# Optimization experiments

Measured on AMD Instinct MI355X. Metric: run time of the kernel, lower is better.

The kernel has to match this reference:

```python
import math
import jax, jax.numpy as jnp
import numpy as np

B, N, M, C, H = 64, 64, 64, 512, 8
HD = C // H
FREQ = 256  # frequency_embedding_size
MAX_PERIOD = 10000.0


def setup_inputs() -> dict:
    key = jax.random.key(0)
    ks = jax.random.split(key, 10)
    s = 1.0 / math.sqrt(C)
    sf = 1.0 / math.sqrt(FREQ)
    return {
        "query": jax.random.normal(ks[0], (B, N, C), jnp.float32),
        "query_pos": jax.random.uniform(ks[1], (1, N, M), jnp.float32),
        # projection weights stored as [in, out]
        "Wq": jax.random.normal(ks[2], (C, C), jnp.float32) * s,
        "bq": jnp.zeros((C,), jnp.float32),
        "Wk": jax.random.normal(ks[3], (C, C), jnp.float32) * s,  # no bias
        "Wv": jax.random.normal(ks[4], (C, C), jnp.float32) * s,
        "bv": jnp.zeros((C,), jnp.float32),
        "Wo": jax.random.normal(ks[5], (C, C), jnp.float32) * s,
        "bo": jnp.zeros((C,), jnp.float32),
        # ScalarEmbedder MLP: Linear(FREQ->C), SiLU, Linear(C->C)
        "W1": jax.random.normal(ks[6], (FREQ, C), jnp.float32) * sf,
        "b1": jnp.zeros((C,), jnp.float32),
        "W2": jax.random.normal(ks[7], (C, C), jnp.float32) * s,
        "b2": jnp.zeros((C,), jnp.float32),
    }


def _freqs():
    half = FREQ // 2
    return jnp.exp(-math.log(MAX_PERIOD) * jnp.arange(half, dtype=jnp.float32) / half)


def reference(query, query_pos, Wq, bq, Wk, Wv, bv, Wo, bo, W1, b1, W2, b2):
    Bq, Nq, Cq = query.shape
    Mk = query_pos.shape[-1]
    # --- ScalarEmbedder on flattened pairwise positions: [N*M] -> [N*M, C]
    t = query_pos.reshape(-1)                       # [Bp*N*M], Bp = 1
    tf = t[:, None] * _freqs()[None, :]             # [N*M, FREQ/2]
    emb = jnp.concatenate([jnp.cos(tf), jnp.sin(tf)], axis=-1)  # [N*M, FREQ]
    pe = jax.nn.silu(emb @ W1 + b1) @ W2 + b2        # [N*M, C]
    pe = pe.reshape(Nq, Mk, H, HD).transpose(2, 0, 1, 3)  # [H, N, M, hd] (tiled over B via broadcast)

    q = (query @ Wq + bq).reshape(Bq, Nq, H, HD)     # bnhd
    k = (query @ Wk).reshape(Bq, Mk, H, HD)          # bmhd (key = query)
    v = (query @ Wv + bv).reshape(Bq, Mk, H, HD)

    scale = HD ** -0.5
    # attn[b,h,n,m] = sum_d q[b,n,h,d] * pe[h,n,m,d] * k[b,m,h,d]
    scores = jnp.einsum("bnhd,hnmd,bmhd->bhnm", q, pe, k) * scale
    attn = jax.nn.softmax(scores, axis=-1)
    x = jnp.einsum("bhnm,bmhd->bnhd", attn, v).reshape(Bq, Nq, Cq)
    return x @ Wo + bo + query  # identity = query
```

## Files before the change

### kernel.cpp

```cpp
#include <hip/hip_runtime.h>
#include <hip/hip_bf16.h>
#include <math.h>

typedef short short8 __attribute__((ext_vector_type(8)));
typedef float floatx4 __attribute__((ext_vector_type(4)));

__device__ __forceinline__ ushort f2bf(float f) {
    __hip_bfloat16 h = __float2bfloat16(f);
    return *reinterpret_cast<ushort*>(&h);
}
__device__ __forceinline__ void bf8_to_f32(uint4 u, float* f) {
    f[0] = __uint_as_float(u.x << 16); f[1] = __uint_as_float(u.x & 0xffff0000u);
    f[2] = __uint_as_float(u.y << 16); f[3] = __uint_as_float(u.y & 0xffff0000u);
    f[4] = __uint_as_float(u.z << 16); f[5] = __uint_as_float(u.z & 0xffff0000u);
    f[6] = __uint_as_float(u.w << 16); f[7] = __uint_as_float(u.w & 0xffff0000u);
}

#define GLDS16(g, l) __builtin_amdgcn_global_load_lds( \
    (const __attribute__((address_space(1))) void*)(g), \
    (__attribute__((address_space(3))) void*)(l), 16, 0, 0)

__global__ __launch_bounds__(256) void prep_kernel(
        const float* __restrict__ W1, const float* __restrict__ W2,
        const float* __restrict__ Wq, const float* __restrict__ Wk,
        const float* __restrict__ Wv, const float* __restrict__ Wo,
        const float* __restrict__ bq, const float* __restrict__ bv,
        const float* __restrict__ query, const float* __restrict__ qpos,
        ushort* __restrict__ W1t, ushort* __restrict__ W2t,
        ushort* __restrict__ Wqkvt, ushort* __restrict__ Wot,
        ushort* __restrict__ queryB, ushort* __restrict__ embB,
        float* __restrict__ biasC) {
    const int z = blockIdx.z;
    const int tx = threadIdx.x, ty = threadIdx.y;
    const int tid = ty * 32 + tx;
    if (z < 6) {
        const float* src; ushort* dst; int R;
        switch (z) {
            case 0:  src = W1; dst = W1t;              R = 256; break;
            case 1:  src = W2; dst = W2t;              R = 512; break;
            case 2:  src = Wq; dst = Wqkvt;            R = 512; break;
            case 3:  src = Wk; dst = Wqkvt + 512*512;  R = 512; break;
            case 4:  src = Wv; dst = Wqkvt + 1024*512; R = 512; break;
            default: src = Wo; dst = Wot;              R = 512; break;
        }
        const int r0 = blockIdx.y * 32, c0 = blockIdx.x * 32;
        if (r0 >= R) return;
        __shared__ float t[32][33];
        for (int i = ty; i < 32; i += 8) t[i][tx] = src[(size_t)(r0 + i) * 512 + c0 + tx];
        __syncthreads();
        for (int i = ty; i < 32; i += 8) dst[(size_t)(c0 + i) * R + r0 + tx] = f2bf(t[tx][i]);
    } else if (z == 6) {
        const int bid = blockIdx.y * 16 + blockIdx.x;
#pragma unroll
        for (int i = 0; i < 8; ++i) {
            size_t idx4 = (size_t)bid * 2048 + i * 256 + tid;
            float4 v = *(const float4*)(query + idx4 * 4);
            ushort4 o; o.x = f2bf(v.x); o.y = f2bf(v.y); o.z = f2bf(v.z); o.w = f2bf(v.w);
            *(ushort4*)(queryB + idx4 * 4) = o;
        }
        if (bid == 0) {
            for (int i = tid; i < 1536; i += 256)
                biasC[i] = (i < 512) ? bq[i] : ((i < 1024) ? 0.0f : bv[i - 1024]);
        }
    } else {
        const int bid = blockIdx.y * 16 + blockIdx.x;
        const int gt = bid * 256 + tid;
        const int e0 = gt * 16;
        const int r = e0 >> 8, j0 = e0 & 255;
        const float t = qpos[r];
        ushort o[16];
#pragma unroll
        for (int u = 0; u < 16; ++u) {
            int j = j0 + u, i = j & 127;
            float freq = __expf(-9.210340371976184f * (float)i * (1.0f / 128.0f));
            float a = t * freq;
            o[u] = f2bf((j < 128) ? __cosf(a) : __sinf(a));
        }
        *(uint4*)(embB + e0)     = *(uint4*)&o[0];
        *(uint4*)(embB + e0 + 8) = *(uint4*)&o[8];
    }
}

template<int BM, int BN>
__global__ __launch_bounds__(256) void gemm_bf16(
        const ushort* __restrict__ A, const ushort* __restrict__ Bt,
        const float* __restrict__ bias, const float* __restrict__ resid,
        void* __restrict__ Cout, int M, int N, int K, int act, int out_fp32) {
    constexpr int MR = BM / 32;
    constexpr int NR = BN / 32;
    __shared__ ushort As[BM * 32];
    __shared__ ushort Bs[BN * 32];
    const int tid = threadIdx.x;
    const int l = tid & 63, w = tid >> 6;
    const int wr = w >> 1, wc = w & 1;
    const int row0 = blockIdx.x * BM, col0 = blockIdx.y * BN;
    const int l15 = l & 15, quad = l >> 4;

    const int srow = tid >> 2;
    const int skoff = (tid & 3) * 8;
    const ushort* gA = A  + (size_t)(row0 + srow) * K + skoff;
    const ushort* gB = Bt + (size_t)(col0 + srow) * K + skoff;

    floatx4 acc[MR][NR] = {};

    for (int k0 = 0; k0 < K; k0 += 32) {
        __syncthreads();
#pragma unroll
        for (int i = 0; i < BM / 64; ++i)
            GLDS16(gA + (size_t)(i * 64) * K + k0, &As[(i * 256 + tid) * 8]);
#pragma unroll
        for (int i = 0; i < BN / 64; ++i)
            GLDS16(gB + (size_t)(i * 64) * K + k0, &Bs[(i * 256 + tid) * 8]);
        __syncthreads();
        short8 af[MR], bf[NR];
#pragma unroll
        for (int m = 0; m < MR; ++m)
            af[m] = *(const short8*)&As[(wr * (BM / 2) + m * 16 + l15) * 32 + quad * 8];
#pragma unroll
        for (int n = 0; n < NR; ++n)
            bf[n] = *(const short8*)&Bs[(wc * (BN / 2) + n * 16 + l15) * 32 + quad * 8];
#pragma unroll
        for (int m = 0; m < MR; ++m)
#pragma unroll
            for (int n = 0; n < NR; ++n)
                acc[m][n] = __builtin_amdgcn_mfma_f32_16x16x32_bf16(af[m], bf[n], acc[m][n], 0, 0, 0);
    }

#pragma unroll
    for (int m = 0; m < MR; ++m)
#pragma unroll
        for (int n = 0; n < NR; ++n) {
            int col = col0 + wc * (BN / 2) + n * 16 + l15;
            float bvv = bias ? bias[col] : 0.0f;
#pragma unroll
            for (int r = 0; r < 4; ++r) {
                int row = row0 + wr * (BM / 2) + m * 16 + quad * 4 + r;
                float val = acc[m][n][r] + bvv;
                if (act) val = val / (1.0f + __expf(-val));
                if (out_fp32) {
                    float rv = resid ? resid[(size_t)row * N + col] : 0.0f;
                    ((float*)Cout)[(size_t)row * N + col] = val + rv;
                } else {
                    ((ushort*)Cout)[(size_t)row * N + col] = f2bf(val);
                }
            }
        }
}

__global__ __launch_bounds__(256) void attn_bf16(
        const ushort* __restrict__ qkv, const ushort* __restrict__ peB,
        ushort* __restrict__ xB) {
    const int h = blockIdx.x, b = blockIdx.y, nh = blockIdx.z;
    const int tid = threadIdx.x;
    const int w = tid >> 6, l = tid & 63;
    const int lo = l & 7, hi = l >> 3;

    __shared__ float ks[64 * 64];
    __shared__ float vs[64 * 64];
    __shared__ float qs[32 * 64];

#pragma unroll
    for (int p = 0; p < 2; ++p) {
        int cid = p * 256 + tid;
        int row = cid >> 3, ch = cid & 7;
        const ushort* base = qkv + (size_t)(b * 64 + row) * 1536 + h * 64 + ch * 8;
        uint4 ku = *(const uint4*)(base + 512);
        uint4 vu = *(const uint4*)(base + 1024);
        float kf[8], vf[8];
        bf8_to_f32(ku, kf); bf8_to_f32(vu, vf);
#pragma unroll
        for (int j = 0; j < 8; ++j) {
            ks[row * 64 + ch * 8 + j] = kf[j];
            vs[row * 64 + ch * 8 + j] = vf[j];
        }
    }
    {
        int row = tid >> 3, ch = tid & 7;
        uint4 qu = *(const uint4*)(qkv + (size_t)(b * 64 + nh * 32 + row) * 1536 + h * 64 + ch * 8);
        float qf[8]; bf8_to_f32(qu, qf);
#pragma unroll
        for (int j = 0; j < 8; ++j) qs[row * 64 + ch * 8 + j] = qf[j];
    }
    __syncthreads();

    for (int i = 0; i < 8; ++i) {
        int nl = w + 4 * i;
        int n = nh * 32 + nl;
        float qf[8];
        *(float4*)&qf[0] = *(const float4*)&qs[nl * 64 + lo * 8];
        *(float4*)&qf[4] = *(const float4*)&qs[nl * 64 + lo * 8 + 4];

        float sreg[8];
#pragma unroll
        for (int mg = 0; mg < 8; ++mg) {
            int m = mg * 8 + hi;
            uint4 pu = *(const uint4*)(peB + (size_t)(n * 64 + m) * 512 + h * 64 + lo * 8);
            float pf[8]; bf8_to_f32(pu, pf);
            float kf[8];
            *(float4*)&kf[0] = *(const float4*)&ks[m * 64 + lo * 8];
            *(float4*)&kf[4] = *(const float4*)&ks[m * 64 + lo * 8 + 4];
            float p = 0.0f;
#pragma unroll
            for (int j = 0; j < 8; ++j) p = fmaf(qf[j] * kf[j], pf[j], p);
            p += __shfl_xor(p, 1);
            p += __shfl_xor(p, 2);
            p += __shfl_xor(p, 4);
            sreg[mg] = p * 0.125f;
        }

        float mx = sreg[0];
#pragma unroll
        for (int mg = 1; mg < 8; ++mg) mx = fmaxf(mx, sreg[mg]);
        mx = fmaxf(mx, __shfl_xor(mx, 8));
        mx = fmaxf(mx, __shfl_xor(mx, 16));
        mx = fmaxf(mx, __shfl_xor(mx, 32));
        float sum = 0.0f;
#pragma unroll
        for (int mg = 0; mg < 8; ++mg) { sreg[mg] = __expf(sreg[mg] - mx); sum += sreg[mg]; }
        sum += __shfl_xor(sum, 8);
        sum += __shfl_xor(sum, 16);
        sum += __shfl_xor(sum, 32);
        float rs = 1.0f / sum;

        float acc[8] = {};
#pragma unroll
        for (int mg = 0; mg < 8; ++mg) {
            int m = mg * 8 + hi;
            float at = sreg[mg] * rs;
            float vf[8];
            *(float4*)&vf[0] = *(const float4*)&vs[m * 64 + lo * 8];
            *(float4*)&vf[4] = *(const float4*)&vs[m * 64 + lo * 8 + 4];
#pragma unroll
            for (int j = 0; j < 8; ++j) acc[j] = fmaf(at, vf[j], acc[j]);
        }
#pragma unroll
        for (int j = 0; j < 8; ++j) {
            acc[j] += __shfl_xor(acc[j], 8);
            acc[j] += __shfl_xor(acc[j], 16);
            acc[j] += __shfl_xor(acc[j], 32);
        }
        if (l < 8) {
            uint4 o;
            o.x = f2bf(acc[0]) | ((uint)f2bf(acc[1]) << 16);
            o.y = f2bf(acc[2]) | ((uint)f2bf(acc[3]) << 16);
            o.z = f2bf(acc[4]) | ((uint)f2bf(acc[5]) << 16);
            o.w = f2bf(acc[6]) | ((uint)f2bf(acc[7]) << 16);
            *(uint4*)(xB + (size_t)(b * 64 + n) * 512 + h * 64 + l * 8) = o;
        }
    }
}

extern "C" void kernel_launch(void* const* d_in, const int* in_sizes, int n_in,
                              void* d_out, int out_size, void* d_ws, size_t ws_size,
                              hipStream_t stream) {
    const float* query = (const float*)d_in[0];
    const float* qpos  = (const float*)d_in[1];
    const float* Wq    = (const float*)d_in[2];
    const float* bq    = (const float*)d_in[3];
    const float* Wk    = (const float*)d_in[4];
    const float* Wv    = (const float*)d_in[5];
    const float* bv    = (const float*)d_in[6];
    const float* Wo    = (const float*)d_in[7];
    const float* bo    = (const float*)d_in[8];
    const float* W1    = (const float*)d_in[9];
    const float* b1    = (const float*)d_in[10];
    const float* W2    = (const float*)d_in[11];
    const float* b2    = (const float*)d_in[12];
    float* out = (float*)d_out;
    char* ws = (char*)d_ws;

    ushort* W1t    = (ushort*)(ws + 0);
    ushort* W2t    = (ushort*)(ws + 262144);
    ushort* Wqkvt  = (ushort*)(ws + 786432);
    ushort* Wot    = (ushort*)(ws + 2359296);
    float*  biasC  = (float*) (ws + 2883584);
    ushort* embB   = (ushort*)(ws + 3145728);
    ushort* queryB = (ushort*)(ws + 5242880);
    ushort* hiddenB= (ushort*)(ws + 9437184);
    ushort* peB    = (ushort*)(ws + 13631488);
    ushort* qkvB   = (ushort*)(ws + 17825792);
    ushort* xB     = (ushort*)(ws + 30408704);

    prep_kernel<<<dim3(16, 16, 8), dim3(32, 8), 0, stream>>>(
        W1, W2, Wq, Wk, Wv, Wo, bq, bv, query, qpos,
        W1t, W2t, Wqkvt, Wot, queryB, embB, biasC);

    gemm_bf16<128, 64><<<dim3(32, 8),  256, 0, stream>>>(embB,    W1t,   b1,    nullptr, hiddenB, 4096,  512, 256, 1, 0);
    gemm_bf16<128, 64><<<dim3(32, 8),  256, 0, stream>>>(hiddenB, W2t,   b2,    nullptr, peB,     4096,  512, 512, 0, 0);
    gemm_bf16<128,128><<<dim3(32, 12), 256, 0, stream>>>(queryB,  Wqkvt, biasC, nullptr, qkvB,    4096, 1536, 512, 0, 0);

    attn_bf16<<<dim3(8, 64, 2), 256, 0, stream>>>(qkvB, peB, xB);

    gemm_bf16<128, 64><<<dim3(32, 8),  256, 0, stream>>>(xB, Wot, bo, query, out, 4096, 512, 512, 0, 1);
}
```

Before: 183.7 us.

## Double-buffer GEMM LDS tiles and co-launch W2 and QKV GEMMs in one grid

Replaces the GEMM kernel with a multi-problem variant whose K loop double-buffers the LDS tiles. The next tile's global-to-LDS load is issued before the MFMAs on the current tile, so only one barrier is needed per iteration. The independent W2 (positional MLP) and QKV projection GEMMs are merged into a single 1024-block launch selected by block index, which fills the GPU better and removes one launch. The QKV GEMM now uses 128x64 tiles instead of 128x128, and LDS use doubles for the second buffer.

```diff
diff --git a/kernel.cpp b/kernel.cpp
--- a/kernel.cpp
+++ b/kernel.cpp
@@ -81,49 +81,65 @@
     }
 }
 
+struct GArgs {
+    const ushort* A; const ushort* Bt; const float* bias; const float* resid;
+    void* C; int N, K, act, outf32, ntn;
+};
+
 template<int BM, int BN>
-__global__ __launch_bounds__(256) void gemm_bf16(
-        const ushort* __restrict__ A, const ushort* __restrict__ Bt,
-        const float* __restrict__ bias, const float* __restrict__ resid,
-        void* __restrict__ Cout, int M, int N, int K, int act, int out_fp32) {
+__global__ __launch_bounds__(256) void gemm_multi(GArgs g0, GArgs g1, int split) {
     constexpr int MR = BM / 32;
     constexpr int NR = BN / 32;
-    __shared__ ushort As[BM * 32];
-    __shared__ ushort Bs[BN * 32];
+    __shared__ ushort As[2][BM * 32];
+    __shared__ ushort Bs[2][BN * 32];
+
+    const bool sel = ((int)blockIdx.x >= split);
+    const GArgs g = sel ? g1 : g0;
+    const int bid = sel ? ((int)blockIdx.x - split) : (int)blockIdx.x;
+    const int tm = bid / g.ntn, tn = bid % g.ntn;
+    const int row0 = tm * BM, col0 = tn * BN;
+    const int K = g.K, N = g.N;
+
     const int tid = threadIdx.x;
     const int l = tid & 63, w = tid >> 6;
     const int wr = w >> 1, wc = w & 1;
-    const int row0 = blockIdx.x * BM, col0 = blockIdx.y * BN;
     const int l15 = l & 15, quad = l >> 4;
 
     const int srow = tid >> 2;
     const int skoff = (tid & 3) * 8;
-    const ushort* gA = A  + (size_t)(row0 + srow) * K + skoff;
-    const ushort* gB = Bt + (size_t)(col0 + srow) * K + skoff;
+    const ushort* gA = g.A  + (size_t)(row0 + srow) * K + skoff;
+    const ushort* gB = g.Bt + (size_t)(col0 + srow) * K + skoff;
+
+    auto stage = [&](int s, int k0) {
+#pragma unroll
+        for (int i = 0; i < BM / 64; ++i)
+            GLDS16(gA + (size_t)(i * 64) * K + k0, &As[s][(i * 256 + tid) * 8]);
+#pragma unroll
+        for (int i = 0; i < BN / 64; ++i)
+            GLDS16(gB + (size_t)(i * 64) * K + k0, &Bs[s][(i * 256 + tid) * 8]);
+    };
 
     floatx4 acc[MR][NR] = {};
 
-    for (int k0 = 0; k0 < K; k0 += 32) {
+    const int nk = K >> 5;
+    stage(0, 0);
+    int cur = 0;
+    for (int t = 0; t < nk; ++t) {
         __syncthreads();
-#pragma unroll
-        for (int i = 0; i < BM / 64; ++i)
-            GLDS16(gA + (size_t)(i * 64) * K + k0, &As[(i * 256 + tid) * 8]);
-#pragma unroll
-        for (int i = 0; i < BN / 64; ++i)
-            GLDS16(gB + (size_t)(i * 64) * K + k0, &Bs[(i * 256 + tid) * 8]);
-        __syncthreads();
+        if (t + 1 < nk) stage(cur ^ 1, (t + 1) * 32);
         short8 af[MR], bf[NR];
 #pragma unroll
         for (int m = 0; m < MR; ++m)
-            af[m] = *(const short8*)&As[(wr * (BM / 2) + m * 16 + l15) * 32 + quad * 8];
+            af[m] = *(const short8*)&As[cur][(wr * (BM / 2) + m * 16 + l15) * 32 + quad * 8];
 #pragma unroll
         for (int n = 0; n < NR; ++n)
-            bf[n] = *(const short8*)&Bs[(wc * (BN / 2) + n * 16 + l15) * 32 + quad * 8];
+            bf[n] = *(const short8*)&Bs[cur][(wc * (BN / 2) + n * 16 + l15) * 32 + quad * 8];
 #pragma unroll
         for (int m = 0; m < MR; ++m)
 #pragma unroll
             for (int n = 0; n < NR; ++n)
                 acc[m][n] = __builtin_amdgcn_mfma_f32_16x16x32_bf16(af[m], bf[n], acc[m][n], 0, 0, 0);
+        cur ^= 1;
     }
 
 #pragma unroll
@@ -131,17 +147,17 @@
 #pragma unroll
         for (int n = 0; n < NR; ++n) {
             int col = col0 + wc * (BN / 2) + n * 16 + l15;
-            float bvv = bias ? bias[col] : 0.0f;
+            float bvv = g.bias ? g.bias[col] : 0.0f;
 #pragma unroll
             for (int r = 0; r < 4; ++r) {
                 int row = row0 + wr * (BM / 2) + m * 16 + quad * 4 + r;
                 float val = acc[m][n][r] + bvv;
-                if (act) val = val / (1.0f + __expf(-val));
-                if (out_fp32) {
-                    float rv = resid ? resid[(size_t)row * N + col] : 0.0f;
-                    ((float*)Cout)[(size_t)row * N + col] = val + rv;
+                if (g.act) val = val / (1.0f + __expf(-val));
+                if (g.outf32) {
+                    float rv = g.resid ? g.resid[(size_t)row * N + col] : 0.0f;
+                    ((float*)g.C)[(size_t)row * N + col] = val + rv;
                 } else {
-                    ((ushort*)Cout)[(size_t)row * N + col] = f2bf(val);
+                    ((ushort*)g.C)[(size_t)row * N + col] = f2bf(val);
                 }
             }
         }
@@ -285,11 +301,15 @@
         W1, W2, Wq, Wk, Wv, Wo, bq, bv, query, qpos,
         W1t, W2t, Wqkvt, Wot, queryB, embB, biasC);
 
-    gemm_bf16<128, 64><<<dim3(32, 8),  256, 0, stream>>>(embB,    W1t,   b1,    nullptr, hiddenB, 4096,  512, 256, 1, 0);
-    gemm_bf16<128, 64><<<dim3(32, 8),  256, 0, stream>>>(hiddenB, W2t,   b2,    nullptr, peB,     4096,  512, 512, 0, 0);
-    gemm_bf16<128,128><<<dim3(32, 12), 256, 0, stream>>>(queryB,  Wqkvt, biasC, nullptr, qkvB,    4096, 1536, 512, 0, 0);
+    GArgs a_g1 { embB,    W1t,   b1,    nullptr, hiddenB, 512,  256, 1, 0, 8  };
+    GArgs a_g2 { hiddenB, W2t,   b2,    nullptr, peB,     512,  512, 0, 0, 8  };
+    GArgs a_qkv{ queryB,  Wqkvt, biasC, nullptr, qkvB,    1536, 512, 0, 0, 24 };
+    GArgs a_out{ xB,      Wot,   bo,    query,   out,     512,  512, 0, 1, 8  };
+
+    gemm_multi<128, 64><<<256, 256, 0, stream>>>(a_g1, a_g1, 1 << 30);
+    gemm_multi<128, 64><<<1024, 256, 0, stream>>>(a_g2, a_qkv, 256);
 
     attn_bf16<<<dim3(8, 64, 2), 256, 0, stream>>>(qkvB, peB, xB);
 
-    gemm_bf16<128, 64><<<dim3(32, 8),  256, 0, stream>>>(xB, Wot, bo, query, out, 4096, 512, 512, 0, 1);
-}
+    gemm_multi<128, 64><<<256, 256, 0, stream>>>(a_out, a_out, 1 << 30);
+}
```

New measurement: 171.2 us. 1.07x faster.

## Fuse all stages into one persistent kernel with grid barriers

Applied to the files above, without the earlier changes.

Replaces the six separate launches with a single persistent kernel of 512 blocks that walks through the prep, GEMM, attention and output stages, separated by atomic-counter grid barriers. It also overlaps the W1 GEMM with the QKV GEMM in one phase, double-buffers the GEMM K-loop LDS staging, pads the attention LDS rows and prefetches the pe loads. The aim is to remove launch gaps and idle tails between stages. In exchange, the grid barriers require all 512 blocks to be co-resident, some stages switch to smaller 64x64 tiles, and a memset is added before the launch.

```diff
diff --git a/kernel.cpp b/kernel.cpp
--- a/kernel.cpp
+++ b/kernel.cpp
@@ -4,6 +4,8 @@
 
 typedef short short8 __attribute__((ext_vector_type(8)));
 typedef float floatx4 __attribute__((ext_vector_type(4)));
+
+#define NBLK 512
 
 __device__ __forceinline__ ushort f2bf(float f) {
     __hip_bfloat16 h = __float2bfloat16(f);
@@ -20,80 +22,101 @@
     (const __attribute__((address_space(1))) void*)(g), \
     (__attribute__((address_space(3))) void*)(l), 16, 0, 0)
 
-__global__ __launch_bounds__(256) void prep_kernel(
-        const float* __restrict__ W1, const float* __restrict__ W2,
-        const float* __restrict__ Wq, const float* __restrict__ Wk,
-        const float* __restrict__ Wv, const float* __restrict__ Wo,
-        const float* __restrict__ bq, const float* __restrict__ bv,
-        const float* __restrict__ query, const float* __restrict__ qpos,
-        ushort* __restrict__ W1t, ushort* __restrict__ W2t,
-        ushort* __restrict__ Wqkvt, ushort* __restrict__ Wot,
-        ushort* __restrict__ queryB, ushort* __restrict__ embB,
-        float* __restrict__ biasC) {
-    const int z = blockIdx.z;
-    const int tx = threadIdx.x, ty = threadIdx.y;
-    const int tid = ty * 32 + tx;
-    if (z < 6) {
-        const float* src; ushort* dst; int R;
-        switch (z) {
-            case 0:  src = W1; dst = W1t;              R = 256; break;
-            case 1:  src = W2; dst = W2t;              R = 512; break;
-            case 2:  src = Wq; dst = Wqkvt;            R = 512; break;
-            case 3:  src = Wk; dst = Wqkvt + 512*512;  R = 512; break;
-            case 4:  src = Wv; dst = Wqkvt + 1024*512; R = 512; break;
-            default: src = Wo; dst = Wot;              R = 512; break;
-        }
-        const int r0 = blockIdx.y * 32, c0 = blockIdx.x * 32;
-        if (r0 >= R) return;
-        __shared__ float t[32][33];
-        for (int i = ty; i < 32; i += 8) t[i][tx] = src[(size_t)(r0 + i) * 512 + c0 + tx];
-        __syncthreads();
-        for (int i = ty; i < 32; i += 8) dst[(size_t)(c0 + i) * R + r0 + tx] = f2bf(t[tx][i]);
-    } else if (z == 6) {
-        const int bid = blockIdx.y * 16 + blockIdx.x;
-#pragma unroll
-        for (int i = 0; i < 8; ++i) {
-            size_t idx4 = (size_t)bid * 2048 + i * 256 + tid;
-            float4 v = *(const float4*)(query + idx4 * 4);
-            ushort4 o; o.x = f2bf(v.x); o.y = f2bf(v.y); o.z = f2bf(v.z); o.w = f2bf(v.w);
-            *(ushort4*)(queryB + idx4 * 4) = o;
-        }
-        if (bid == 0) {
-            for (int i = tid; i < 1536; i += 256)
-                biasC[i] = (i < 512) ? bq[i] : ((i < 1024) ? 0.0f : bv[i - 1024]);
-        }
-    } else {
-        const int bid = blockIdx.y * 16 + blockIdx.x;
-        const int gt = bid * 256 + tid;
-        const int e0 = gt * 16;
-        const int r = e0 >> 8, j0 = e0 & 255;
-        const float t = qpos[r];
-        ushort o[16];
-#pragma unroll
-        for (int u = 0; u < 16; ++u) {
-            int j = j0 + u, i = j & 127;
-            float freq = __expf(-9.210340371976184f * (float)i * (1.0f / 128.0f));
-            float a = t * freq;
-            o[u] = f2bf((j < 128) ? __cosf(a) : __sinf(a));
-        }
-        *(uint4*)(embB + e0)     = *(uint4*)&o[0];
-        *(uint4*)(embB + e0 + 8) = *(uint4*)&o[8];
-    }
+__device__ __forceinline__ void gbar(uint* cnt, uint target) {
+    __syncthreads();
+    __threadfence();
+    if (threadIdx.x == 0) {
+        __hip_atomic_fetch_add(cnt, 1u, __ATOMIC_ACQ_REL, __HIP_MEMORY_SCOPE_AGENT);
+        uint v;
+        do {
+            __builtin_amdgcn_s_sleep(1);
+            v = __hip_atomic_load(cnt, __ATOMIC_ACQUIRE, __HIP_MEMORY_SCOPE_AGENT);
+        } while (v < target);
+    }
+    __syncthreads();
+    __threadfence();
+}
+
+struct FusedArgs {
+    const float *W1, *W2, *Wq, *Wk, *Wv, *Wo, *bq, *bv, *bo, *b1, *b2;
+    const float *query, *qpos;
+    ushort *W1t, *W2t, *Wqkvt, *Wot, *queryB, *embB;
+    float *biasC;
+    ushort *hiddenB, *peB, *qkvB, *xB;
+    float *out;
+    uint *bars;
+};
+
+__device__ void transpose_task(int t, const FusedArgs& a, char* smem) {
+    const float* src; ushort* dst; int R, z, by, bx;
+    if (t < 128) { z = 0; by = t >> 4; bx = t & 15; }
+    else { int u = t - 128; z = 1 + (u >> 8); int idx = u & 255; by = idx >> 4; bx = idx & 15; }
+    switch (z) {
+        case 0:  src = a.W1; dst = a.W1t;                R = 256; break;
+        case 1:  src = a.W2; dst = a.W2t;                R = 512; break;
+        case 2:  src = a.Wq; dst = a.Wqkvt;              R = 512; break;
+        case 3:  src = a.Wk; dst = a.Wqkvt + 512 * 512;  R = 512; break;
+        case 4:  src = a.Wv; dst = a.Wqkvt + 1024 * 512; R = 512; break;
+        default: src = a.Wo; dst = a.Wot;                R = 512; break;
+    }
+    const int r0 = by * 32, c0 = bx * 32;
+    const int tid = threadIdx.x;
+    const int tx = tid & 31, ty = tid >> 5;
+    float* tt = (float*)smem;
+    __syncthreads();
+    for (int i = ty; i < 32; i += 8) tt[i * 33 + tx] = src[(size_t)(r0 + i) * 512 + c0 + tx];
+    __syncthreads();
+    for (int i = ty; i < 32; i += 8) dst[(size_t)(c0 + i) * R + r0 + tx] = f2bf(tt[tx * 33 + i]);
+}
+
+__device__ void qcast_task(int bid, const FusedArgs& a) {
+    const int tid = threadIdx.x;
+#pragma unroll
+    for (int i = 0; i < 8; ++i) {
+        size_t idx4 = (size_t)bid * 2048 + i * 256 + tid;
+        float4 v = *(const float4*)(a.query + idx4 * 4);
+        ushort4 o; o.x = f2bf(v.x); o.y = f2bf(v.y); o.z = f2bf(v.z); o.w = f2bf(v.w);
+        *(ushort4*)(a.queryB + idx4 * 4) = o;
+    }
+    if (bid == 0) {
+        for (int i = tid; i < 1536; i += 256)
+            a.biasC[i] = (i < 512) ? a.bq[i] : ((i < 1024) ? 0.0f : a.bv[i - 1024]);
+    }
+}
+
+__device__ void emb_task(int bid, const FusedArgs& a) {
+    const int tid = threadIdx.x;
+    const int gt = bid * 256 + tid;
+    const int e0 = gt * 16;
+    const int r = e0 >> 8, j0 = e0 & 255;
+    const float t = a.qpos[r];
+    ushort o[16];
+#pragma unroll
+    for (int u = 0; u < 16; ++u) {
+        int j = j0 + u, i = j & 127;
+        float freq = __expf(-9.210340371976184f * (float)i * (1.0f / 128.0f));
+        float ang = t * freq;
+        o[u] = f2bf((j < 128) ? __cosf(ang) : __sinf(ang));
+    }
+    *(uint4*)(a.embB + e0)     = *(uint4*)&o[0];
+    *(uint4*)(a.embB + e0 + 8) = *(uint4*)&o[8];
 }
 
 template<int BM, int BN>
-__global__ __launch_bounds__(256) void gemm_bf16(
-        const ushort* __restrict__ A, const ushort* __restrict__ Bt,
-        const float* __restrict__ bias, const float* __restrict__ resid,
-        void* __restrict__ Cout, int M, int N, int K, int act, int out_fp32) {
+__device__ void gemm_tile(const ushort* __restrict__ A, const ushort* __restrict__ Bt,
+                          const float* __restrict__ bias, const float* __restrict__ resid,
+                          void* __restrict__ Cout, int N, int K, int act, int outf32,
+                          int ntn, int bid, char* smem) {
     constexpr int MR = BM / 32;
     constexpr int NR = BN / 32;
-    __shared__ ushort As[BM * 32];
-    __shared__ ushort Bs[BN * 32];
+    ushort* As = (ushort*)smem;
+    ushort* Bs = As + 2 * BM * 32;
+    const int tm = bid / ntn, tn = bid % ntn;
+    const int row0 = tm * BM, col0 = tn * BN;
+
     const int tid = threadIdx.x;
     const int l = tid & 63, w = tid >> 6;
     const int wr = w >> 1, wc = w & 1;
-    const int row0 = blockIdx.x * BM, col0 = blockIdx.y * BN;
     const int l15 = l & 15, quad = l >> 4;
 
     const int srow = tid >> 2;
@@ -101,29 +124,38 @@
     const ushort* gA = A  + (size_t)(row0 + srow) * K + skoff;
     const ushort* gB = Bt + (size_t)(col0 + srow) * K + skoff;
 
+    auto stage = [&](int s, int k0) {
+#pragma unroll
+        for (int i = 0; i < BM / 64; ++i)
+            GLDS16(gA + (size_t)(i * 64) * K + k0, &As[(size_t)s * BM * 32 + (i * 256 + tid) * 8]);
+#pragma unroll
+        for (int i = 0; i < BN / 64; ++i)
+            GLDS16(gB + (size_t)(i * 64) * K + k0, &Bs[(size_t)s * BN * 32 + (i * 256 + tid) * 8]);
+    };
+
     floatx4 acc[MR][NR] = {};
-
-    for (int k0 = 0; k0 < K; k0 += 32) {
+    const int nk = K >> 5;
+    __syncthreads();
+    stage(0, 0);
+    int cur = 0;
+    for (int t = 0; t < nk; ++t) {
         __syncthreads();
-#pragma unroll
-        for (int i = 0; i < BM / 64; ++i)
-            GLDS16(gA + (size_t)(i * 64) * K + k0, &As[(i * 256 + tid) * 8]);
-#pragma unroll
-        for (int i = 0; i < BN / 64; ++i)
-            GLDS16(gB + (size_t)(i * 64) * K + k0, &Bs[(i * 256 + tid) * 8]);
-        __syncthreads();
+        if (t + 1 < nk) stage(cur ^ 1, (t + 1) * 32);
+        const ushort* Ab = As + (size_t)cur * BM * 32;
+        const ushort* Bb = Bs + (size_t)cur * BN * 32;
         short8 af[MR], bf[NR];
 #pragma unroll
         for (int m = 0; m < MR; ++m)
-            af[m] = *(const short8*)&As[(wr * (BM / 2) + m * 16 + l15) * 32 + quad * 8];
+            af[m] = *(const short8*)&Ab[(wr * (BM / 2) + m * 16 + l15) * 32 + quad * 8];
 #pragma unroll
         for (int n = 0; n < NR; ++n)
-            bf[n] = *(const short8*)&Bs[(wc * (BN / 2) + n * 16 + l15) * 32 + quad * 8];
+            bf[n] = *(const short8*)&Bb[(wc * (BN / 2) + n * 16 + l15) * 32 + quad * 8];
 #pragma unroll
         for (int m = 0; m < MR; ++m)
 #pragma unroll
             for (int n = 0; n < NR; ++n)
                 acc[m][n] = __builtin_amdgcn_mfma_f32_16x16x32_bf16(af[m], bf[n], acc[m][n], 0, 0, 0);
+        cur ^= 1;
     }
 
 #pragma unroll
@@ -137,7 +169,7 @@
                 int row = row0 + wr * (BM / 2) + m * 16 + quad * 4 + r;
                 float val = acc[m][n][r] + bvv;
                 if (act) val = val / (1.0f + __expf(-val));
-                if (out_fp32) {
+                if (outf32) {
                     float rv = resid ? resid[(size_t)row * N + col] : 0.0f;
                     ((float*)Cout)[(size_t)row * N + col] = val + rv;
                 } else {
@@ -147,18 +179,17 @@
         }
 }
 
-__global__ __launch_bounds__(256) void attn_bf16(
-        const ushort* __restrict__ qkv, const ushort* __restrict__ peB,
-        ushort* __restrict__ xB) {
-    const int h = blockIdx.x, b = blockIdx.y, nh = blockIdx.z;
+__device__ void attn_unit(const ushort* __restrict__ qkv, const ushort* __restrict__ peB,
+                          ushort* __restrict__ xB, int h, int b, int nh, char* smem) {
+    constexpr int LP = 68;
+    float* ks = (float*)smem;
+    float* vs = ks + 64 * LP;
+    float* qs = vs + 64 * LP;
     const int tid = threadIdx.x;
     const int w = tid >> 6, l = tid & 63;
     const int lo = l & 7, hi = l >> 3;
 
-    __shared__ float ks[64 * 64];
-    __shared__ float vs[64 * 64];
-    __shared__ float qs[32 * 64];
-
+    __syncthreads();
 #pragma unroll
     for (int p = 0; p < 2; ++p) {
         int cid = p * 256 + tid;
@@ -170,8 +201,8 @@
         bf8_to_f32(ku, kf); bf8_to_f32(vu, vf);
 #pragma unroll
         for (int j = 0; j < 8; ++j) {
-            ks[row * 64 + ch * 8 + j] = kf[j];
-            vs[row * 64 + ch * 8 + j] = vf[j];
+            ks[row * LP + ch * 8 + j] = kf[j];
+            vs[row * LP + ch * 8 + j] = vf[j];
         }
     }
     {
@@ -179,7 +210,7 @@
         uint4 qu = *(const uint4*)(qkv + (size_t)(b * 64 + nh * 32 + row) * 1536 + h * 64 + ch * 8);
         float qf[8]; bf8_to_f32(qu, qf);
 #pragma unroll
-        for (int j = 0; j < 8; ++j) qs[row * 64 + ch * 8 + j] = qf[j];
+        for (int j = 0; j < 8; ++j) qs[row * LP + ch * 8 + j] = qf[j];
     }
     __syncthreads();
 
@@ -187,18 +218,22 @@
         int nl = w + 4 * i;
         int n = nh * 32 + nl;
         float qf[8];
-        *(float4*)&qf[0] = *(const float4*)&qs[nl * 64 + lo * 8];
-        *(float4*)&qf[4] = *(const float4*)&qs[nl * 64 + lo * 8 + 4];
+        *(float4*)&qf[0] = *(const float4*)&qs[nl * LP + lo * 8];
+        *(float4*)&qf[4] = *(const float4*)&qs[nl * LP + lo * 8 + 4];
+
+        uint4 pu[8];
+#pragma unroll
+        for (int mg = 0; mg < 8; ++mg)
+            pu[mg] = *(const uint4*)(peB + (size_t)(n * 64 + mg * 8 + hi) * 512 + h * 64 + lo * 8);
 
         float sreg[8];
 #pragma unroll
         for (int mg = 0; mg < 8; ++mg) {
             int m = mg * 8 + hi;
-            uint4 pu = *(const uint4*)(peB + (size_t)(n * 64 + m) * 512 + h * 64 + lo * 8);
-            float pf[8]; bf8_to_f32(pu, pf);
+            float pf[8]; bf8_to_f32(pu[mg], pf);
             float kf[8];
-            *(float4*)&kf[0] = *(const float4*)&ks[m * 64 + lo * 8];
-            *(float4*)&kf[4] = *(const float4*)&ks[m * 64 + lo * 8 + 4];
+            *(float4*)&kf[0] = *(const float4*)&ks[m * LP + lo * 8];
+            *(float4*)&kf[4] = *(const float4*)&ks[m * LP + lo * 8 + 4];
             float p = 0.0f;
 #pragma unroll
             for (int j = 0; j < 8; ++j) p = fmaf(qf[j] * kf[j], pf[j], p);
@@ -228,8 +263,8 @@
             int m = mg * 8 + hi;
             float at = sreg[mg] * rs;
             float vf[8];
-            *(float4*)&vf[0] = *(const float4*)&vs[m * 64 + lo * 8];
-            *(float4*)&vf[4] = *(const float4*)&vs[m * 64 + lo * 8 + 4];
+            *(float4*)&vf[0] = *(const float4*)&vs[m * LP + lo * 8];
+            *(float4*)&vf[4] = *(const float4*)&vs[m * LP + lo * 8 + 4];
 #pragma unroll
             for (int j = 0; j < 8; ++j) acc[j] = fmaf(at, vf[j], acc[j]);
         }
@@ -250,46 +285,76 @@
     }
 }
 
+__global__ __launch_bounds__(256, 2) void fused_all(FusedArgs a) {
+    __shared__ __align__(16) char smem[43520];
+    const int blk = blockIdx.x;
+
+    for (int task = blk; task < 1920; task += NBLK) {
+        if (task < 1408)      transpose_task(task, a, smem);
+        else if (task < 1664) qcast_task(task - 1408, a);
+        else                  emb_task(task - 1664, a);
+    }
+    gbar(a.bars + 0, NBLK);
+
+    for (int rep = 0; rep < 2; ++rep) {
+        int id = blk + rep * NBLK;
+        if (id < 256)
+            gemm_tile<128, 64>(a.embB, a.W1t, a.b1, nullptr, a.hiddenB,
+                               512, 256, 1, 0, 8, id, smem);
+        else
+            gemm_tile<128, 64>(a.queryB, a.Wqkvt, a.biasC, nullptr, a.qkvB,
+                               1536, 512, 0, 0, 24, id - 256, smem);
+    }
+    gbar(a.bars + 32, NBLK);
+
+    gemm_tile<64, 64>(a.hiddenB, a.W2t, a.b2, nullptr, a.peB,
+                      512, 512, 0, 0, 8, blk, smem);
+    gbar(a.bars + 64, NBLK);
+
+    for (int rep = 0; rep < 2; ++rep) {
+        int u = blk + rep * NBLK;
+        attn_unit(a.qkvB, a.peB, a.xB, u & 7, (u >> 3) & 63, u >> 9, smem);
+    }
+    gbar(a.bars + 96, NBLK);
+
+    gemm_tile<64, 64>(a.xB, a.Wot, a.bo, a.query, a.out,
+                      512, 512, 0, 1, 8, blk, smem);
+}
+
 extern "C" void kernel_launch(void* const* d_in, const int* in_sizes, int n_in,
                               void* d_out, int out_size, void* d_ws, size_t ws_size,
                               hipStream_t stream) {
-    const float* query = (const float*)d_in[0];
-    const float* qpos  = (const float*)d_in[1];
-    const float* Wq    = (const float*)d_in[2];
-    const float* bq    = (const float*)d_in[3];
-    const float* Wk    = (const float*)d_in[4];
-    const float* Wv    = (const float*)d_in[5];
-    const float* bv    = (const float*)d_in[6];
-    const float* Wo    = (const float*)d_in[7];
-    const float* bo    = (const float*)d_in[8];
-    const float* W1    = (const float*)d_in[9];
-    const float* b1    = (const float*)d_in[10];
-    const float* W2    = (const float*)d_in[11];
-    const float* b2    = (const float*)d_in[12];
-    float* out = (float*)d_out;
     char* ws = (char*)d_ws;
 
-    ushort* W1t    = (ushort*)(ws + 0);
-    ushort* W2t    = (ushort*)(ws + 262144);
-    ushort* Wqkvt  = (ushort*)(ws + 786432);
-    ushort* Wot    = (ushort*)(ws + 2359296);
-    float*  biasC  = (float*) (ws + 2883584);
-    ushort* embB   = (ushort*)(ws + 3145728);
-    ushort* queryB = (ushort*)(ws + 5242880);
-    ushort* hiddenB= (ushort*)(ws + 9437184);
-    ushort* peB    = (ushort*)(ws + 13631488);
-    ushort* qkvB   = (ushort*)(ws + 17825792);
-    ushort* xB     = (ushort*)(ws + 30408704);
-
-    prep_kernel<<<dim3(16, 16, 8), dim3(32, 8), 0, stream>>>(
-        W1, W2, Wq, Wk, Wv, Wo, bq, bv, query, qpos,
-        W1t, W2t, Wqkvt, Wot, queryB, embB, biasC);
-
-    gemm_bf16<128, 64><<<dim3(32, 8),  256, 0, stream>>>(embB,    W1t,   b1,    nullptr, hiddenB, 4096,  512, 256, 1, 0);
-    gemm_bf16<128, 64><<<dim3(32, 8),  256, 0, stream>>>(hiddenB, W2t,   b2,    nullptr, peB,     4096,  512, 512, 0, 0);
-    gemm_bf16<128,128><<<dim3(32, 12), 256, 0, stream>>>(queryB,  Wqkvt, biasC, nullptr, qkvB,    4096, 1536, 512, 0, 0);
-
-    attn_bf16<<<dim3(8, 64, 2), 256, 0, stream>>>(qkvB, peB, xB);
-
-    gemm_bf16<128, 64><<<dim3(32, 8),  256, 0, stream>>>(xB, Wot, bo, query, out, 4096, 512, 512, 0, 1);
-}
+    FusedArgs fa;
+    fa.query = (const float*)d_in[0];
+    fa.qpos  = (const float*)d_in[1];
+    fa.Wq    = (const float*)d_in[2];
+    fa.bq    = (const float*)d_in[3];
+    fa.Wk    = (const float*)d_in[4];
+    fa.Wv    = (const float*)d_in[5];
+    fa.bv    = (const float*)d_in[6];
+    fa.Wo    = (const float*)d_in[7];
+    fa.bo    = (const float*)d_in[8];
+    fa.W1    = (const float*)d_in[9];
+    fa.b1    = (const float*)d_in[10];
+    fa.W2    = (const float*)d_in[11];
+    fa.b2    = (const float*)d_in[12];
+    fa.out   = (float*)d_out;
+
+    fa.W1t    = (ushort*)(ws + 0);
+    fa.W2t    = (ushort*)(ws + 262144);
+    fa.Wqkvt  = (ushort*)(ws + 786432);
+    fa.Wot    = (ushort*)(ws + 2359296);
+    fa.biasC  = (float*) (ws + 2883584);
+    fa.embB   = (ushort*)(ws + 3145728);
+    fa.queryB = (ushort*)(ws + 5242880);
+    fa.hiddenB= (ushort*)(ws + 9437184);
+    fa.peB    = (ushort*)(ws + 13631488);
+    fa.qkvB   = (ushort*)(ws + 17825792);
+    fa.xB     = (ushort*)(ws + 30408704);
+    fa.bars   = (uint*)  (ws + 34603008);
+
+    hipMemsetAsync(fa.bars, 0, 512, stream);
+    fused_all<<<NBLK, 256, 0, stream>>>(fa);
+}
```

Result: slower. 627.3 us (+241.5%).
